# Performance work log

Measured on AMD Instinct MI355X. Metric: run time of the kernel, lower is better.

## Reference

```python
import jax, jax.numpy as jnp
import numpy as np

VAR_WEIGHT = 1.0
DIST_WEIGHT = 1.0
MARGIN_VAR = 0.5
MARGIN_DIST = 3.0
IGNORE_LABEL = 255
MAX_INST = 12  # static C: max instance id present in gt (labels 1..12, 0=background)


def setup_inputs() -> dict:
    key = jax.random.key(0)
    k1, k2 = jax.random.split(key)
    featmap = jax.random.normal(k1, (8, 16, 368, 640), dtype=jnp.float32)
    gt = jax.random.randint(k2, (8, 1, 368, 640), 0, 13, dtype=jnp.int64)
    return {"featmap": featmap, "gt": gt}


def _push_pull_loss(featmap, gt):
    B, N, H, W = featmap.shape
    P = H * W
    feat = featmap.reshape(B, N, P)                      # [B,N,P]
    labels = gt.reshape(B, P)                            # [B,P] int
    ids = jnp.arange(1, MAX_INST + 1)                    # instance ids 1..C
    # one-hot instance masks  [B,C,P]
    mask = (labels[:, None, :] == ids[None, :, None]).astype(feat.dtype)
    counts = mask.sum(axis=-1)                           # [B,C]
    present = counts > 0                                 # [B,C]
    safe_counts = jnp.maximum(counts, 1.0)
    # per-instance centers (segment mean)  [B,C,N]
    centers = jnp.einsum('bnp,bcp->bcn', feat, mask) / safe_counts[:, :, None]

    # --- pull: per-pixel distance to own-instance center ---
    feat_sq = jnp.sum(feat * feat, axis=1)               # [B,P]
    cen_sq = jnp.sum(centers * centers, axis=-1)         # [B,C]
    cross = jnp.einsum('bcn,bnp->bcp', centers, feat)    # [B,C,P]
    sq = feat_sq[:, None, :] + cen_sq[:, :, None] - 2.0 * cross
    sq = jnp.maximum(sq, 0.0)
    d = jnp.where(sq > 0, jnp.sqrt(jnp.where(sq > 0, sq, 1.0)), 0.0)  # [B,C,P]
    hinge = jnp.maximum(d - MARGIN_VAR, 0.0)
    # per-instance mean over its own pixels
    inst_pull = jnp.sum(hinge * mask, axis=-1) / safe_counts          # [B,C]
    n_inst = jnp.sum(present.astype(feat.dtype))
    pull_loss = jnp.where(
        n_inst > 0,
        jnp.sum(jnp.where(present, inst_pull, 0.0)) / jnp.maximum(n_inst, 1.0),
        0.0 * feat.mean(),
    ) * VAR_WEIGHT

    # --- push: pairwise center distances within each batch sample ---
    diff = centers[:, :, None, :] - centers[:, None, :, :]            # [B,C,C,N]
    psq = jnp.sum(diff * diff, axis=-1)                               # [B,C,C]
    pd = jnp.where(psq > 0, jnp.sqrt(jnp.where(psq > 0, psq, 1.0)), 0.0)
    pair_valid = (present[:, :, None] & present[:, None, :] &
                  (~jnp.eye(MAX_INST, dtype=bool))[None]).astype(feat.dtype)
    push_vals = jnp.maximum(2.0 * MARGIN_DIST - pd, 0.0)
    n_pairs = jnp.sum(pair_valid)
    push_loss = jnp.where(
        n_pairs > 0,
        jnp.sum(push_vals * pair_valid) / jnp.maximum(n_pairs, 1.0),
        0.0 * feat.mean(),
    ) * DIST_WEIGHT

    return push_loss + pull_loss


def reference(featmap, gt):
    return _push_pull_loss(featmap, gt)
```

## Files before the change

### kernel.cpp

```cpp
#include <hip/hip_runtime.h>
#include <hip/hip_bf16.h>

constexpr int B_ = 8;
constexpr int N_ = 16;
constexpr int H_ = 368;
constexpr int W_ = 640;
constexpr int P_ = H_ * W_;
constexpr int C_ = 12;
constexpr float MARGIN_VAR_ = 0.5f;
constexpr float MARGIN_DIST_ = 3.0f;

constexpr int OFF_SUMS = 0;
constexpr int OFF_CNT  = OFF_SUMS + B_*C_*N_;
constexpr int WS_FLOATS = OFF_CNT + B_*C_;

constexpr int TPB = 256;

constexpr int MCHUNK = 1024;
constexpr int MBPI   = P_ / MCHUNK;
constexpr int PCHUNK = 1024;
constexpr int PBPI   = P_ / PCHUNK;

typedef short bf16x8 __attribute__((ext_vector_type(8)));
typedef float f32x4  __attribute__((ext_vector_type(4)));

__device__ __forceinline__ short f2bf(float f) {
    __hip_bfloat16 h = __float2bfloat16(f);
    return __builtin_bit_cast(short, h);
}

__global__ __launch_bounds__(TPB) void k_accum(const float* __restrict__ feat,
                                               const int* __restrict__ gt,
                                               float* __restrict__ ws,
                                               float* __restrict__ out) {
    __shared__ int   s_lab[MCHUNK];
    __shared__ float s_red[4][C_];
    __shared__ float s_fin[4][256];

    const int tid  = threadIdx.x;
    const int lane = tid & 63, wid = tid >> 6;
    const int b     = blockIdx.x / MBPI;
    const int chunk = blockIdx.x % MBPI;
    const int base  = chunk * MCHUNK;

    if (blockIdx.x == 0 && tid == 0) out[0] = 0.f;

    const int*   __restrict__ gb = gt   + (size_t)b * P_ + base;
    const float* __restrict__ fb = feat + (size_t)b * N_ * P_ + base;

    const int4 la = ((const int4*)gb)[tid];
    ((int4*)s_lab)[tid] = la;

    float cnt[C_];
    #pragma unroll
    for (int c = 0; c < C_; ++c) {
        cnt[c] = ((la.x == c+1) ? 1.f : 0.f) + ((la.y == c+1) ? 1.f : 0.f)
               + ((la.z == c+1) ? 1.f : 0.f) + ((la.w == c+1) ? 1.f : 0.f);
    }
    #pragma unroll
    for (int off = 32; off > 0; off >>= 1) {
        #pragma unroll
        for (int c = 0; c < C_; ++c) cnt[c] += __shfl_xor(cnt[c], off, 64);
    }
    if (lane == 0) {
        #pragma unroll
        for (int c = 0; c < C_; ++c) s_red[wid][c] = cnt[c];
    }
    __syncthreads();
    if (tid < C_) {
        const float t = s_red[0][tid] + s_red[1][tid] + s_red[2][tid] + s_red[3][tid];
        atomicAdd(&ws[OFF_CNT + b * C_ + tid], t);
    }

    const int n     = lane & 15;
    const int cls   = n + 1;
    const int ko    = (lane >> 4) * 8;
    const int wbase = wid * 256;
    const float* __restrict__ fp = fb + (size_t)n * P_;

    f32x4 acc = {0.f, 0.f, 0.f, 0.f};

    float4 ra[2], rb[2];
    ra[0] = *(const float4*)(fp + wbase + 0 * 32 + ko);
    rb[0] = *(const float4*)(fp + wbase + 0 * 32 + ko + 4);
    ra[1] = *(const float4*)(fp + wbase + 1 * 32 + ko);
    rb[1] = *(const float4*)(fp + wbase + 1 * 32 + ko + 4);

    #pragma unroll
    for (int t = 0; t < 8; ++t) {
        const int s = t & 1;
        const float4 c0 = ra[s], c1 = rb[s];
        if (t < 6) {
            ra[s] = *(const float4*)(fp + wbase + (t + 2) * 32 + ko);
            rb[s] = *(const float4*)(fp + wbase + (t + 2) * 32 + ko + 4);
        }
        const int* lp = s_lab + wbase + t * 32 + ko;
        const int4 L0 = *(const int4*)(lp);
        const int4 L1 = *(const int4*)(lp + 4);

        bf16x8 afrag, bfrag;
        afrag[0] = (L0.x == cls) ? (short)0x3F80 : (short)0;
        afrag[1] = (L0.y == cls) ? (short)0x3F80 : (short)0;
        afrag[2] = (L0.z == cls) ? (short)0x3F80 : (short)0;
        afrag[3] = (L0.w == cls) ? (short)0x3F80 : (short)0;
        afrag[4] = (L1.x == cls) ? (short)0x3F80 : (short)0;
        afrag[5] = (L1.y == cls) ? (short)0x3F80 : (short)0;
        afrag[6] = (L1.z == cls) ? (short)0x3F80 : (short)0;
        afrag[7] = (L1.w == cls) ? (short)0x3F80 : (short)0;

        bfrag[0] = f2bf(c0.x); bfrag[1] = f2bf(c0.y);
        bfrag[2] = f2bf(c0.z); bfrag[3] = f2bf(c0.w);
        bfrag[4] = f2bf(c1.x); bfrag[5] = f2bf(c1.y);
        bfrag[6] = f2bf(c1.z); bfrag[7] = f2bf(c1.w);

        acc = __builtin_amdgcn_mfma_f32_16x16x32_bf16(afrag, bfrag, acc, 0, 0, 0);
    }

    #pragma unroll
    for (int r = 0; r < 4; ++r) s_fin[wid][lane * 4 + r] = acc[r];
    __syncthreads();

    {
        const float sv = s_fin[0][tid] + s_fin[1][tid] + s_fin[2][tid] + s_fin[3][tid];
        const int elane = tid >> 2, r = tid & 3;
        const int row = (elane >> 4) * 4 + r;
        const int col = elane & 15;
        if (row < C_)
            atomicAdd(&ws[OFF_SUMS + ((size_t)b * C_ + row) * N_ + col], sv);
    }
}

__global__ __launch_bounds__(TPB) void k_pull(const float* __restrict__ feat,
                                              const int* __restrict__ gt,
                                              const float* __restrict__ ws,
                                              float* __restrict__ out) {
    __shared__ float s_cen[C_][N_ + 1];
    __shared__ float s_w[C_];
    __shared__ float s_cntv[B_ * C_];
    __shared__ float red[TPB];
    __shared__ float wsum[TPB / 64];

    const int tid   = threadIdx.x;
    const int b     = blockIdx.x / PBPI;
    const int chunk = blockIdx.x % PBPI;
    const int base  = chunk * PCHUNK;

    const int4 lb = *(const int4*)(gt + (size_t)b * P_ + base + tid * 4);
    float4 v[N_];
    #pragma unroll
    for (int n = 0; n < N_; ++n)
        v[n] = *(const float4*)(feat + ((size_t)b * N_ + n) * P_ + base + tid * 4);

    if (tid < B_ * C_) s_cntv[tid] = ws[OFF_CNT + tid];
    __syncthreads();
    red[tid] = (tid < B_ * C_ && s_cntv[tid] > 0.f) ? 1.f : 0.f;
    __syncthreads();
    for (int s = TPB / 2; s > 0; s >>= 1) {
        if (tid < s) red[tid] += red[tid + s];
        __syncthreads();
    }
    const float n_inst = red[0];
    __syncthreads();

    if (tid < C_ * N_) {
        const int c = tid >> 4, n = tid & 15;
        const float ct = s_cntv[b * C_ + c];
        s_cen[c][n] = ws[OFF_SUMS + ((size_t)b * C_ + c) * N_ + n] / fmaxf(ct, 1.f);
    }
    if (tid < C_) {
        const float ct = s_cntv[b * C_ + tid];
        s_w[tid] = (ct > 0.f && n_inst > 0.f) ? 1.0f / (ct * n_inst) : 0.f;
    }
    __syncthreads();

    if (chunk == 0) {
        float ps = 0.f;
        if (tid < C_ * C_) {
            const int i = tid / C_, j = tid % C_;
            if (i != j && s_cntv[b * C_ + i] > 0.f && s_cntv[b * C_ + j] > 0.f) {
                float sq = 0.f;
                #pragma unroll
                for (int n = 0; n < N_; ++n) {
                    const float d = s_cen[i][n] - s_cen[j][n];
                    sq += d * d;
                }
                ps = fmaxf(2.f * MARGIN_DIST_ - sqrtf(sq), 0.f);
            }
        }
        red[tid] = ps;
        __syncthreads();
        for (int s = TPB / 2; s > 0; s >>= 1) {
            if (tid < s) red[tid] += red[tid + s];
            __syncthreads();
        }
        if (tid == 0) {
            float np = 0.f;
            for (int bb = 0; bb < B_; ++bb) {
                int k = 0;
                for (int c = 0; c < C_; ++c) k += (s_cntv[bb * C_ + c] > 0.f) ? 1 : 0;
                np += (float)(k * (k - 1));
            }
            if (np > 0.f) atomicAdd(out, red[0] / np);
        }
    }

    const bool vx = (lb.x >= 1 && lb.x <= C_);
    const bool vy = (lb.y >= 1 && lb.y <= C_);
    const bool vz = (lb.z >= 1 && lb.z <= C_);
    const bool vw = (lb.w >= 1 && lb.w <= C_);
    const int cx = vx ? lb.x - 1 : 0;
    const int cy = vy ? lb.y - 1 : 0;
    const int cz = vz ? lb.z - 1 : 0;
    const int cw = vw ? lb.w - 1 : 0;

    float sq0 = 0.f, sq1 = 0.f, sq2 = 0.f, sq3 = 0.f;
    #pragma unroll
    for (int n = 0; n < N_; ++n) {
        const float d0 = v[n].x - s_cen[cx][n];
        const float d1 = v[n].y - s_cen[cy][n];
        const float d2 = v[n].z - s_cen[cz][n];
        const float d3 = v[n].w - s_cen[cw][n];
        sq0 += d0 * d0; sq1 += d1 * d1; sq2 += d2 * d2; sq3 += d3 * d3;
    }
    float acc = 0.f;
    acc += fmaxf(sqrtf(sq0) - MARGIN_VAR_, 0.f) * (vx ? s_w[cx] : 0.f);
    acc += fmaxf(sqrtf(sq1) - MARGIN_VAR_, 0.f) * (vy ? s_w[cy] : 0.f);
    acc += fmaxf(sqrtf(sq2) - MARGIN_VAR_, 0.f) * (vz ? s_w[cz] : 0.f);
    acc += fmaxf(sqrtf(sq3) - MARGIN_VAR_, 0.f) * (vw ? s_w[cw] : 0.f);

    #pragma unroll
    for (int off = 32; off > 0; off >>= 1) acc += __shfl_down(acc, off, 64);
    const int lane = tid & 63, wid = tid >> 6;
    if (lane == 0) wsum[wid] = acc;
    __syncthreads();
    if (tid == 0) {
        float t = 0.f;
        #pragma unroll
        for (int w = 0; w < TPB / 64; ++w) t += wsum[w];
        atomicAdd(out, t);
    }
}

extern "C" void kernel_launch(void* const* d_in, const int* in_sizes, int n_in,
                              void* d_out, int out_size, void* d_ws, size_t ws_size,
                              hipStream_t stream) {
    const float* feat = (const float*)d_in[0];
    const int*   gt   = (const int*)d_in[1];
    float* out = (float*)d_out;
    float* ws  = (float*)d_ws;

    hipMemsetAsync(d_ws, 0, WS_FLOATS * sizeof(float), stream);

    k_accum<<<dim3(B_ * MBPI), dim3(TPB), 0, stream>>>(feat, gt, ws, out);
    k_pull <<<dim3(B_ * PBPI), dim3(TPB), 0, stream>>>(feat, gt, ws, out);
}
```

Before: 70.85 us.

## Deepen load prefetch, pack MFMA fragments, and stream pull-kernel feature loads

In the accumulation kernel, the feature prefetch grows from a double buffer to a four-deep buffer, and the bf16 fragments are built as packed 32-bit words instead of per-element short inserts. In the pull kernel, the 16 per-channel float4 loads are split into two 4-register groups that are refilled while earlier groups are consumed, which lowers register pressure. The shared-memory tree reduction for n_inst is replaced by each thread counting all 96 entries itself, which removes several barriers. The aims are better occupancy, more memory-level parallelism and fewer syncs, at the cost of some redundant per-thread work and possibly less load overlap in the pull kernel.

```diff
diff --git a/kernel.cpp b/kernel.cpp
--- a/kernel.cpp
+++ b/kernel.cpp
@@ -24,9 +24,17 @@
 typedef short bf16x8 __attribute__((ext_vector_type(8)));
 typedef float f32x4  __attribute__((ext_vector_type(4)));
 
+union FragU { int4 i; bf16x8 v; };
+
 __device__ __forceinline__ short f2bf(float f) {
     __hip_bfloat16 h = __float2bfloat16(f);
     return __builtin_bit_cast(short, h);
+}
+
+__device__ __forceinline__ int pack_bf2(float x, float y) {
+    const unsigned lo = (unsigned short)f2bf(x);
+    const unsigned hi = (unsigned short)f2bf(y);
+    return (int)(lo | (hi << 16));
 }
 
 __global__ __launch_bounds__(TPB) void k_accum(const float* __restrict__ feat,
@@ -78,42 +86,38 @@
     const int wbase = wid * 256;
     const float* __restrict__ fp = fb + (size_t)n * P_;
 
+    float4 ba[4], bb[4];
+    #pragma unroll
+    for (int t = 0; t < 4; ++t) {
+        ba[t] = *(const float4*)(fp + wbase + t * 32 + ko);
+        bb[t] = *(const float4*)(fp + wbase + t * 32 + ko + 4);
+    }
+
     f32x4 acc = {0.f, 0.f, 0.f, 0.f};
 
-    float4 ra[2], rb[2];
-    ra[0] = *(const float4*)(fp + wbase + 0 * 32 + ko);
-    rb[0] = *(const float4*)(fp + wbase + 0 * 32 + ko + 4);
-    ra[1] = *(const float4*)(fp + wbase + 1 * 32 + ko);
-    rb[1] = *(const float4*)(fp + wbase + 1 * 32 + ko + 4);
-
     #pragma unroll
     for (int t = 0; t < 8; ++t) {
-        const int s = t & 1;
-        const float4 c0 = ra[s], c1 = rb[s];
-        if (t < 6) {
-            ra[s] = *(const float4*)(fp + wbase + (t + 2) * 32 + ko);
-            rb[s] = *(const float4*)(fp + wbase + (t + 2) * 32 + ko + 4);
+        const float4 c0 = ba[t & 3], c1 = bb[t & 3];
+        if (t < 4) {
+            ba[t & 3] = *(const float4*)(fp + wbase + (t + 4) * 32 + ko);
+            bb[t & 3] = *(const float4*)(fp + wbase + (t + 4) * 32 + ko + 4);
         }
         const int* lp = s_lab + wbase + t * 32 + ko;
         const int4 L0 = *(const int4*)(lp);
         const int4 L1 = *(const int4*)(lp + 4);
 
-        bf16x8 afrag, bfrag;
-        afrag[0] = (L0.x == cls) ? (short)0x3F80 : (short)0;
-        afrag[1] = (L0.y == cls) ? (short)0x3F80 : (short)0;
-        afrag[2] = (L0.z == cls) ? (short)0x3F80 : (short)0;
-        afrag[3] = (L0.w == cls) ? (short)0x3F80 : (short)0;
-        afrag[4] = (L1.x == cls) ? (short)0x3F80 : (short)0;
-        afrag[5] = (L1.y == cls) ? (short)0x3F80 : (short)0;
-        afrag[6] = (L1.z == cls) ? (short)0x3F80 : (short)0;
-        afrag[7] = (L1.w == cls) ? (short)0x3F80 : (short)0;
-
-        bfrag[0] = f2bf(c0.x); bfrag[1] = f2bf(c0.y);
-        bfrag[2] = f2bf(c0.z); bfrag[3] = f2bf(c0.w);
-        bfrag[4] = f2bf(c1.x); bfrag[5] = f2bf(c1.y);
-        bfrag[6] = f2bf(c1.z); bfrag[7] = f2bf(c1.w);
-
-        acc = __builtin_amdgcn_mfma_f32_16x16x32_bf16(afrag, bfrag, acc, 0, 0, 0);
+        FragU au, bu;
+        au.i.x = ((L0.x == cls) ? 0x3F80 : 0) | ((L0.y == cls) ? 0x3F800000 : 0);
+        au.i.y = ((L0.z == cls) ? 0x3F80 : 0) | ((L0.w == cls) ? 0x3F800000 : 0);
+        au.i.z = ((L1.x == cls) ? 0x3F80 : 0) | ((L1.y == cls) ? 0x3F800000 : 0);
+        au.i.w = ((L1.z == cls) ? 0x3F80 : 0) | ((L1.w == cls) ? 0x3F800000 : 0);
+
+        bu.i.x = pack_bf2(c0.x, c0.y);
+        bu.i.y = pack_bf2(c0.z, c0.w);
+        bu.i.z = pack_bf2(c1.x, c1.y);
+        bu.i.w = pack_bf2(c1.z, c1.w);
+
+        acc = __builtin_amdgcn_mfma_f32_16x16x32_bf16(au.v, bu.v, acc, 0, 0, 0);
     }
 
     #pragma unroll
@@ -145,22 +149,21 @@
     const int chunk = blockIdx.x % PBPI;
     const int base  = chunk * PCHUNK;
 
+    const float* __restrict__ fbase = feat + (size_t)b * N_ * P_ + base + tid * 4;
+
     const int4 lb = *(const int4*)(gt + (size_t)b * P_ + base + tid * 4);
-    float4 v[N_];
-    #pragma unroll
-    for (int n = 0; n < N_; ++n)
-        v[n] = *(const float4*)(feat + ((size_t)b * N_ + n) * P_ + base + tid * 4);
+    float4 va[4], vb[4];
+    #pragma unroll
+    for (int j = 0; j < 4; ++j) va[j] = *(const float4*)(fbase + (size_t)(j) * P_);
+    #pragma unroll
+    for (int j = 0; j < 4; ++j) vb[j] = *(const float4*)(fbase + (size_t)(4 + j) * P_);
 
     if (tid < B_ * C_) s_cntv[tid] = ws[OFF_CNT + tid];
     __syncthreads();
-    red[tid] = (tid < B_ * C_ && s_cntv[tid] > 0.f) ? 1.f : 0.f;
-    __syncthreads();
-    for (int s = TPB / 2; s > 0; s >>= 1) {
-        if (tid < s) red[tid] += red[tid + s];
-        __syncthreads();
-    }
-    const float n_inst = red[0];
-    __syncthreads();
+
+    float n_inst = 0.f;
+    #pragma unroll 8
+    for (int i = 0; i < B_ * C_; ++i) n_inst += (s_cntv[i] > 0.f) ? 1.f : 0.f;
 
     if (tid < C_ * N_) {
         const int c = tid >> 4, n = tid & 15;
@@ -195,9 +198,9 @@
         }
         if (tid == 0) {
             float np = 0.f;
-            for (int bb = 0; bb < B_; ++bb) {
+            for (int bb_ = 0; bb_ < B_; ++bb_) {
                 int k = 0;
-                for (int c = 0; c < C_; ++c) k += (s_cntv[bb * C_ + c] > 0.f) ? 1 : 0;
+                for (int c = 0; c < C_; ++c) k += (s_cntv[bb_ * C_ + c] > 0.f) ? 1 : 0;
                 np += (float)(k * (k - 1));
             }
             if (np > 0.f) atomicAdd(out, red[0] / np);
@@ -214,14 +217,28 @@
     const int cw = vw ? lb.w - 1 : 0;
 
     float sq0 = 0.f, sq1 = 0.f, sq2 = 0.f, sq3 = 0.f;
-    #pragma unroll
-    for (int n = 0; n < N_; ++n) {
-        const float d0 = v[n].x - s_cen[cx][n];
-        const float d1 = v[n].y - s_cen[cy][n];
-        const float d2 = v[n].z - s_cen[cz][n];
-        const float d3 = v[n].w - s_cen[cw][n];
-        sq0 += d0 * d0; sq1 += d1 * d1; sq2 += d2 * d2; sq3 += d3 * d3;
-    }
+
+    auto consume4 = [&](const float4* r, int cb) {
+        #pragma unroll
+        for (int j = 0; j < 4; ++j) {
+            const int nn = cb + j;
+            const float d0 = r[j].x - s_cen[cx][nn];
+            const float d1 = r[j].y - s_cen[cy][nn];
+            const float d2 = r[j].z - s_cen[cz][nn];
+            const float d3 = r[j].w - s_cen[cw][nn];
+            sq0 += d0 * d0; sq1 += d1 * d1; sq2 += d2 * d2; sq3 += d3 * d3;
+        }
+    };
+
+    consume4(va, 0);
+    #pragma unroll
+    for (int j = 0; j < 4; ++j) va[j] = *(const float4*)(fbase + (size_t)(8 + j) * P_);
+    consume4(vb, 4);
+    #pragma unroll
+    for (int j = 0; j < 4; ++j) vb[j] = *(const float4*)(fbase + (size_t)(12 + j) * P_);
+    consume4(va, 8);
+    consume4(vb, 12);
+
     float acc = 0.f;
     acc += fmaxf(sqrtf(sq0) - MARGIN_VAR_, 0.f) * (vx ? s_w[cx] : 0.f);
     acc += fmaxf(sqrtf(sq1) - MARGIN_VAR_, 0.f) * (vy ? s_w[cy] : 0.f);
@@ -249,7 +266,7 @@
     float* out = (float*)d_out;
     float* ws  = (float*)d_ws;
 
-    hipMemsetAsync(d_ws, 0, WS_FLOATS * sizeof(float), stream);
+    (void)hipMemsetAsync(d_ws, 0, WS_FLOATS * sizeof(float), stream);
 
     k_accum<<<dim3(B_ * MBPI), dim3(TPB), 0, stream>>>(feat, gt, ws, out);
     k_pull <<<dim3(B_ * PBPI), dim3(TPB), 0, stream>>>(feat, gt, ws, out);
```

Measured after the change: 70.49 us. No clear change (-0.5%).
